# Optimization experiments

Measured on AMD Instinct MI355X. Metric: run time of the kernel, lower is better.

## Reference

```python
import jax, jax.numpy as jnp
import numpy as np

B, S, D = 8, 2048, 512
FF = 2048
E = 8

def setup_inputs() -> dict:
    key = jax.random.key(0)
    ks = jax.random.split(key, 7)
    s = 1.0 / np.sqrt(D)
    sf = 1.0 / np.sqrt(FF)
    return {
        "x":  jax.random.normal(ks[0], (B, S, D), dtype=jnp.float32),
        "Wg": jax.random.uniform(ks[1], (D, E), jnp.float32, -s, s),
        "bg": jax.random.uniform(ks[2], (E,), jnp.float32, -s, s),
        "W1": jax.random.uniform(ks[3], (E, D, FF), jnp.float32, -s, s),
        "b1": jax.random.uniform(ks[4], (E, FF), jnp.float32, -s, s),
        "W2": jax.random.uniform(ks[5], (E, FF, D), jnp.float32, -sf, sf),
        "b2": jax.random.uniform(ks[6], (E, D), jnp.float32, -sf, sf),
    }

def reference(x, Wg, bg, W1, b1, W2, b2):
    b, s, d = x.shape
    xf = x.reshape(-1, d)                      # [T, D]
    logits = xf @ Wg + bg                      # [T, E]
    probs = jax.nn.softmax(logits, axis=-1)
    pmax = jnp.max(probs, axis=-1)             # [T]
    routes = jnp.argmax(probs, axis=-1)        # [T] int
    xs = xf * pmax[:, None]                    # scale tokens by router prob
    # per-expert FFN over all tokens, select the routed expert's output
    out_tok = jnp.zeros_like(xf)
    for e in range(E):
        h = jax.nn.relu(xs @ W1[e] + b1[e])    # [T, FF]
        y = h @ W2[e] + b2[e]                  # [T, D]
        out_tok = jnp.where((routes == e)[:, None], y, out_tok)
    # torch.cat of per-expert nonzero-index gathers == tokens stably sorted by expert id
    order = jnp.argsort(routes)                # jnp.argsort is stable
    return out_tok[order].reshape(b, s, d)
```

## Files before the change

kernel.cpp:

```cpp
#include <hip/hip_runtime.h>
#include <hip/hip_bf16.h>

constexpr int TTOK  = 16384;
constexpr int DDIM  = 512;
constexpr int FFDIM = 2048;
constexpr int NEXP  = 8;
constexpr int GB_TOK = 16;
constexpr int NGB    = TTOK / GB_TOK;
constexpr int MAXTILES = TTOK / 128 + NEXP;

typedef __attribute__((ext_vector_type(8))) short short8_t;
typedef __attribute__((ext_vector_type(4))) float f32x4_t;

__device__ __forceinline__ unsigned short f2bf(float f) {
    union { float f; unsigned u; } v; v.f = f;
    return (unsigned short)((v.u + 0x7fffu + ((v.u >> 16) & 1u)) >> 16);
}

__device__ __forceinline__ void gl_lds16(const void* g, void* l) {
    __builtin_amdgcn_global_load_lds(
        (const __attribute__((address_space(1))) void*)g,
        (__attribute__((address_space(3))) void*)l,
        16, 0, 0);
}

__global__ __launch_bounds__(256) void transpose_cvt2(const float* __restrict__ W1,
                                                      const float* __restrict__ W2,
                                                      unsigned short* __restrict__ W1T,
                                                      unsigned short* __restrict__ W2T) {
    __shared__ float tile[32][33];
    int z = blockIdx.z;
    bool isW2 = z >= NEXP;
    int e = isW2 ? z - NEXP : z;
    int R = isW2 ? FFDIM : DDIM;
    int C = isW2 ? DDIM : FFDIM;
    int tilesC = C / 32;
    int t = blockIdx.x;
    int c0 = (t % tilesC) * 32;
    int r0 = (t / tilesC) * 32;
    const float* s = (isW2 ? W2 : W1) + (size_t)e * DDIM * FFDIM;
    unsigned short* d = (isW2 ? W2T : W1T) + (size_t)e * DDIM * FFDIM;
    int tx = threadIdx.x & 31, ty = threadIdx.x >> 5;
    #pragma unroll
    for (int i = 0; i < 4; i++)
        tile[ty + 8 * i][tx] = s[(size_t)(r0 + ty + 8 * i) * C + c0 + tx];
    __syncthreads();
    #pragma unroll
    for (int i = 0; i < 4; i++)
        d[(size_t)(c0 + ty + 8 * i) * R + r0 + tx] = f2bf(tile[tx][ty + 8 * i]);
}

__global__ __launch_bounds__(256) void gate_kernel(const float* __restrict__ x,
                                                   const float* __restrict__ Wg,
                                                   const float* __restrict__ bg,
                                                   int* __restrict__ route,
                                                   float* __restrict__ pmax,
                                                   int* __restrict__ blockCounts) {
    __shared__ int cnt[NEXP];
    __shared__ float bgs[NEXP];
    int tid = threadIdx.x;
    if (tid < NEXP) { cnt[tid] = 0; bgs[tid] = bg[tid]; }
    __syncthreads();
    int wave = tid >> 6, lane = tid & 63;
    float w[8][8];
    #pragma unroll
    for (int jj = 0; jj < 8; jj++) {
        float4 a = *(const float4*)(Wg + (size_t)(lane * 8 + jj) * NEXP);
        float4 b = *(const float4*)(Wg + (size_t)(lane * 8 + jj) * NEXP + 4);
        w[jj][0] = a.x; w[jj][1] = a.y; w[jj][2] = a.z; w[jj][3] = a.w;
        w[jj][4] = b.x; w[jj][5] = b.y; w[jj][6] = b.z; w[jj][7] = b.w;
    }
    int tbase = blockIdx.x * GB_TOK + wave * 4;
    for (int it = 0; it < 4; it++) {
        int t = tbase + it;
        float4 xa = *(const float4*)(x + (size_t)t * DDIM + lane * 8);
        float4 xb = *(const float4*)(x + (size_t)t * DDIM + lane * 8 + 4);
        float xs[8] = {xa.x, xa.y, xa.z, xa.w, xb.x, xb.y, xb.z, xb.w};
        double acc[NEXP];
        #pragma unroll
        for (int e = 0; e < NEXP; e++) acc[e] = 0.0;
        #pragma unroll
        for (int jj = 0; jj < 8; jj++) {
            double xv = (double)xs[jj];
            #pragma unroll
            for (int e = 0; e < NEXP; e++) acc[e] += xv * (double)w[jj][e];
        }
        #pragma unroll
        for (int off = 32; off > 0; off >>= 1) {
            #pragma unroll
            for (int e = 0; e < NEXP; e++) acc[e] += __shfl_down(acc[e], off);
        }
        if (lane == 0) {
            double l[NEXP];
            #pragma unroll
            for (int e = 0; e < NEXP; e++) l[e] = acc[e] + (double)bgs[e];
            int r = 0; double lm = l[0];
            #pragma unroll
            for (int e = 1; e < NEXP; e++) if (l[e] > lm) { lm = l[e]; r = e; }
            double s = 0.0;
            #pragma unroll
            for (int e = 0; e < NEXP; e++) s += exp(l[e] - lm);
            route[t] = r;
            pmax[t] = (float)(1.0 / s);
            atomicAdd(&cnt[r], 1);
        }
    }
    __syncthreads();
    if (tid < NEXP) blockCounts[blockIdx.x * NEXP + tid] = cnt[tid];
}

__global__ __launch_bounds__(1024) void scan_kernel(const int* __restrict__ blockCounts,
                                                    int* __restrict__ blockOffsets,
                                                    int* __restrict__ segPrefix,
                                                    int* __restrict__ tilePrefix) {
    __shared__ int sc[NGB][NEXP];
    __shared__ int base[NEXP + 1];
    int b = threadIdx.x;
    int c[NEXP];
    #pragma unroll
    for (int e = 0; e < NEXP; e++) { c[e] = blockCounts[b * NEXP + e]; sc[b][e] = c[e]; }
    __syncthreads();
    for (int off = 1; off < NGB; off <<= 1) {
        int t[NEXP];
        if (b >= off) {
            #pragma unroll
            for (int e = 0; e < NEXP; e++) t[e] = sc[b - off][e];
        }
        __syncthreads();
        if (b >= off) {
            #pragma unroll
            for (int e = 0; e < NEXP; e++) sc[b][e] += t[e];
        }
        __syncthreads();
    }
    if (b == 0) {
        int s = 0;
        #pragma unroll
        for (int e = 0; e < NEXP; e++) { base[e] = s; s += sc[NGB - 1][e]; }
        base[NEXP] = s;
        for (int e = 0; e <= NEXP; e++) segPrefix[e] = base[e];
        int tp = 0;
        tilePrefix[0] = 0;
        for (int e = 0; e < NEXP; e++) {
            tp += (sc[NGB - 1][e] + 127) / 128;
            tilePrefix[e + 1] = tp;
        }
    }
    __syncthreads();
    #pragma unroll
    for (int e = 0; e < NEXP; e++)
        blockOffsets[b * NEXP + e] = base[e] + sc[b][e] - c[e];
}

__global__ __launch_bounds__(256) void scatter_kernel(const float* __restrict__ x,
                                                      const int* __restrict__ route,
                                                      const float* __restrict__ pmax,
                                                      const int* __restrict__ blockOffsets,
                                                      unsigned short* __restrict__ Xs) {
    __shared__ int dstL[GB_TOK];
    __shared__ float pmL[GB_TOK];
    int tid = threadIdx.x;
    int bb = blockIdx.x;
    if (tid < GB_TOK) {
        int t = bb * GB_TOK + tid;
        int r = route[t];
        unsigned long long ltmask = (tid == 0) ? 0ull : ((~0ull) >> (64 - tid));
        int rank = 0;
        #pragma unroll
        for (int e = 0; e < NEXP; e++) {
            unsigned long long m = __ballot(r == e);
            if (r == e) rank = __popcll(m & ltmask);
        }
        dstL[tid] = blockOffsets[bb * NEXP + r] + rank;
        pmL[tid] = pmax[t];
    }
    __syncthreads();
    int wave = tid >> 6, lane = tid & 63;
    for (int rr = 0; rr < 4; rr++) {
        int rowl = wave * 4 + rr;
        int t = bb * GB_TOK + rowl;
        float pm = pmL[rowl];
        const float4* xr = (const float4*)(x + (size_t)t * DDIM) + lane * 2;
        float4 a = xr[0], b = xr[1];
        union { short8_t v; unsigned short s[8]; } o;
        o.s[0] = f2bf(a.x * pm); o.s[1] = f2bf(a.y * pm);
        o.s[2] = f2bf(a.z * pm); o.s[3] = f2bf(a.w * pm);
        o.s[4] = f2bf(b.x * pm); o.s[5] = f2bf(b.y * pm);
        o.s[6] = f2bf(b.z * pm); o.s[7] = f2bf(b.w * pm);
        *(short8_t*)(Xs + (size_t)dstL[rowl] * DDIM + lane * 8) = o.v;
    }
}

template <bool RELU, typename OutT, int K, int N>
__global__ __launch_bounds__(256) void gemm_seg(const unsigned short* __restrict__ A,
                                                const unsigned short* __restrict__ Bt,
                                                const float* __restrict__ bias,
                                                OutT* __restrict__ C,
                                                const int* __restrict__ segPrefix,
                                                const int* __restrict__ tilePrefix) {
    int t = blockIdx.x;
    if (t >= tilePrefix[NEXP]) return;
    int e = 0;
    #pragma unroll
    for (int i = 1; i <= NEXP; i++) e += (t >= tilePrefix[i]) ? 1 : 0;
    int seg1 = segPrefix[e + 1];
    int m0 = segPrefix[e] + (t - tilePrefix[e]) * 128;
    int n0 = blockIdx.y * 128;

    __shared__ unsigned short As[2 * 4096];
    __shared__ unsigned short Bs[2 * 4096];

    int tid = threadIdx.x, wave = tid >> 6, lane = tid & 63;
    const unsigned short* Bte = Bt + (size_t)e * N * K;

    int srow = lane >> 2;
    int sg   = (lane & 3) ^ ((lane >> 2) & 3) ^ ((lane >> 4) & 3);
    int scol = sg * 8;

    f32x4_t acc[4][4];
    #pragma unroll
    for (int i = 0; i < 4; i++)
        #pragma unroll
        for (int j = 0; j < 4; j++) acc[i][j] = (f32x4_t){0.f, 0.f, 0.f, 0.f};

    int wm = (wave & 1) * 64;
    int wn = (wave >> 1) * 64;
    int frow = lane & 15;
    int gr = lane >> 4;
    int fswz = (gr ^ (frow & 3) ^ ((frow >> 2) & 3)) * 8;

    int reg0 = wave * 2;
    int arow0 = m0 + reg0 * 16 + srow;
    arow0 = arow0 < TTOK ? arow0 : TTOK - 1;
    int arow1 = m0 + (reg0 + 1) * 16 + srow;
    arow1 = arow1 < TTOK ? arow1 : TTOK - 1;
    const unsigned short* aptr0 = A + (size_t)arow0 * K + scol;
    const unsigned short* aptr1 = A + (size_t)arow1 * K + scol;
    const unsigned short* bptr0 = Bte + (size_t)(n0 + reg0 * 16 + srow) * K + scol;
    const unsigned short* bptr1 = Bte + (size_t)(n0 + (reg0 + 1) * 16 + srow) * K + scol;

    #pragma unroll
    for (int kc = 0; kc < K; kc += 64) {
        #pragma unroll
        for (int p = 0; p < 2; p++) {
            gl_lds16(aptr0 + kc + p * 32, &As[p * 4096 + reg0 * 512]);
            gl_lds16(aptr1 + kc + p * 32, &As[p * 4096 + (reg0 + 1) * 512]);
            gl_lds16(bptr0 + kc + p * 32, &Bs[p * 4096 + reg0 * 512]);
            gl_lds16(bptr1 + kc + p * 32, &Bs[p * 4096 + (reg0 + 1) * 512]);
        }
        __syncthreads();
        #pragma unroll
        for (int p = 0; p < 2; p++) {
            short8_t af[4], bfr[4];
            #pragma unroll
            for (int i = 0; i < 4; i++)
                af[i] = *(const short8_t*)&As[p * 4096 + (wm + i * 16 + frow) * 32 + fswz];
            #pragma unroll
            for (int j = 0; j < 4; j++)
                bfr[j] = *(const short8_t*)&Bs[p * 4096 + (wn + j * 16 + frow) * 32 + fswz];
            #pragma unroll
            for (int i = 0; i < 4; i++)
                #pragma unroll
                for (int j = 0; j < 4; j++)
                    acc[i][j] = __builtin_amdgcn_mfma_f32_16x16x32_bf16(af[i], bfr[j], acc[i][j], 0, 0, 0);
        }
        __syncthreads();
    }

    int quad = lane >> 4;
    int colb = lane & 15;
    float bv[4];
    #pragma unroll
    for (int j = 0; j < 4; j++) bv[j] = bias[(size_t)e * N + n0 + wn + j * 16 + colb];

    if constexpr (sizeof(OutT) == 2) {
        unsigned short* cbuf = As;
        #pragma unroll
        for (int p = 0; p < 2; p++) {
            __syncthreads();
            if ((wave >> 1) == p) {
                #pragma unroll
                for (int i = 0; i < 4; i++)
                    #pragma unroll
                    for (int j = 0; j < 4; j++)
                        #pragma unroll
                        for (int r = 0; r < 4; r++) {
                            float v = acc[i][j][r] + bv[j];
                            if (RELU) v = fmaxf(v, 0.0f);
                            cbuf[(wm + i * 16 + quad * 4 + r) * 72 + j * 16 + colb] = f2bf(v);
                        }
            }
            __syncthreads();
            int row = tid >> 1, ch = (tid & 1) * 32;
            int grow = m0 + row;
            if (grow < seg1) {
                #pragma unroll
                for (int k = 0; k < 4; k++) {
                    short8_t v = *(const short8_t*)&cbuf[row * 72 + ch + k * 8];
                    *(short8_t*)&C[(size_t)grow * N + n0 + p * 64 + ch + k * 8] = v;
                }
            }
        }
    } else {
        #pragma unroll
        for (int i = 0; i < 4; i++) {
            #pragma unroll
            for (int j = 0; j < 4; j++) {
                int col = n0 + wn + j * 16 + colb;
                #pragma unroll
                for (int r = 0; r < 4; r++) {
                    int row = m0 + wm + i * 16 + quad * 4 + r;
                    if (row < seg1) {
                        float v = acc[i][j][r] + bv[j];
                        if (RELU) v = fmaxf(v, 0.0f);
                        C[(size_t)row * N + col] = v;
                    }
                }
            }
        }
    }
}

extern "C" void kernel_launch(void* const* d_in, const int* in_sizes, int n_in,
                              void* d_out, int out_size, void* d_ws, size_t ws_size,
                              hipStream_t stream) {
    const float* x  = (const float*)d_in[0];
    const float* Wg = (const float*)d_in[1];
    const float* bg = (const float*)d_in[2];
    const float* W1 = (const float*)d_in[3];
    const float* b1 = (const float*)d_in[4];
    const float* W2 = (const float*)d_in[5];
    const float* b2 = (const float*)d_in[6];
    float* out = (float*)d_out;

    char* ws = (char*)d_ws;
    size_t off = 0;
    auto alloc = [&](size_t bytes) -> char* {
        char* p = ws + off;
        off += (bytes + 255) & ~(size_t)255;
        return p;
    };
    unsigned short* W1T = (unsigned short*)alloc((size_t)NEXP * DDIM * FFDIM * 2);
    unsigned short* W2T = (unsigned short*)alloc((size_t)NEXP * DDIM * FFDIM * 2);
    unsigned short* Xs  = (unsigned short*)alloc((size_t)TTOK * DDIM * 2);
    unsigned short* H   = (unsigned short*)alloc((size_t)TTOK * FFDIM * 2);
    int*   route        = (int*)alloc((size_t)TTOK * 4);
    float* pmaxArr      = (float*)alloc((size_t)TTOK * 4);
    int*   blockCounts  = (int*)alloc((size_t)NGB * NEXP * 4);
    int*   blockOffsets = (int*)alloc((size_t)NGB * NEXP * 4);
    int*   segPrefix    = (int*)alloc((size_t)(NEXP + 1) * 4);
    int*   tilePrefix   = (int*)alloc((size_t)(NEXP + 1) * 4);

    transpose_cvt2<<<dim3(1024, 1, 2 * NEXP), 256, 0, stream>>>(W1, W2, W1T, W2T);
    gate_kernel<<<NGB, 256, 0, stream>>>(x, Wg, bg, route, pmaxArr, blockCounts);
    scan_kernel<<<1, NGB, 0, stream>>>(blockCounts, blockOffsets, segPrefix, tilePrefix);
    scatter_kernel<<<NGB, 256, 0, stream>>>(x, route, pmaxArr, blockOffsets, Xs);
    gemm_seg<true, unsigned short, DDIM, FFDIM><<<dim3(MAXTILES, FFDIM / 128, 1), 256, 0, stream>>>(
        Xs, W1T, b1, H, segPrefix, tilePrefix);
    gemm_seg<false, float, FFDIM, DDIM><<<dim3(MAXTILES, DDIM / 128, 1), 256, 0, stream>>>(
        H, W2T, b2, out, segPrefix, tilePrefix);
}
```

Measured before the change: 311.5 us.

## Double-buffer LDS tiles in expert GEMM, swizzle tile order and epilogue LDS

Doubles the shared-memory A/B buffers so the next K-chunk is loaded via global_load_lds while the current chunk feeds the MFMAs. This leaves one barrier per iteration instead of two and is meant to hide global load latency. It also remaps blockIdx.x to interleave tiles across groups of eight, and XOR-swizzles the bf16 epilogue staging buffer to cut LDS bank conflicts. LDS use per block doubles to 64 KB, which may lower occupancy. The async LDS loads are not explicitly waited on before the barrier, so correctness relies on the compiler inserting the waits.

```diff
diff --git a/kernel.cpp b/kernel.cpp
--- a/kernel.cpp
+++ b/kernel.cpp
@@ -198,7 +198,9 @@
                                                 OutT* __restrict__ C,
                                                 const int* __restrict__ segPrefix,
                                                 const int* __restrict__ tilePrefix) {
-    int t = blockIdx.x;
+    int bx = blockIdx.x;
+    bx = (bx & 7) * (MAXTILES / 8) + (bx >> 3);
+    int t = bx;
     if (t >= tilePrefix[NEXP]) return;
     int e = 0;
     #pragma unroll
@@ -207,8 +209,8 @@
     int m0 = segPrefix[e] + (t - tilePrefix[e]) * 128;
     int n0 = blockIdx.y * 128;
 
-    __shared__ unsigned short As[2 * 4096];
-    __shared__ unsigned short Bs[2 * 4096];
+    __shared__ unsigned short As[2 * 8192];
+    __shared__ unsigned short Bs[2 * 8192];
 
     int tid = threadIdx.x, wave = tid >> 6, lane = tid & 63;
     const unsigned short* Bte = Bt + (size_t)e * N * K;
@@ -239,33 +241,44 @@
     const unsigned short* bptr0 = Bte + (size_t)(n0 + reg0 * 16 + srow) * K + scol;
     const unsigned short* bptr1 = Bte + (size_t)(n0 + (reg0 + 1) * 16 + srow) * K + scol;
 
-    #pragma unroll
-    for (int kc = 0; kc < K; kc += 64) {
+    auto stage = [&](int buf, int kc) {
+        int lb = buf * 8192 + reg0 * 512;
         #pragma unroll
         for (int p = 0; p < 2; p++) {
-            gl_lds16(aptr0 + kc + p * 32, &As[p * 4096 + reg0 * 512]);
-            gl_lds16(aptr1 + kc + p * 32, &As[p * 4096 + (reg0 + 1) * 512]);
-            gl_lds16(bptr0 + kc + p * 32, &Bs[p * 4096 + reg0 * 512]);
-            gl_lds16(bptr1 + kc + p * 32, &Bs[p * 4096 + (reg0 + 1) * 512]);
-        }
-        __syncthreads();
+            gl_lds16(aptr0 + kc + p * 32, &As[lb + p * 4096]);
+            gl_lds16(aptr1 + kc + p * 32, &As[lb + p * 4096 + 512]);
+            gl_lds16(bptr0 + kc + p * 32, &Bs[lb + p * 4096]);
+            gl_lds16(bptr1 + kc + p * 32, &Bs[lb + p * 4096 + 512]);
+        }
+    };
+    auto compute = [&](int buf) {
         #pragma unroll
         for (int p = 0; p < 2; p++) {
             short8_t af[4], bfr[4];
             #pragma unroll
             for (int i = 0; i < 4; i++)
-                af[i] = *(const short8_t*)&As[p * 4096 + (wm + i * 16 + frow) * 32 + fswz];
+                af[i] = *(const short8_t*)&As[buf * 8192 + p * 4096 + (wm + i * 16 + frow) * 32 + fswz];
             #pragma unroll
             for (int j = 0; j < 4; j++)
-                bfr[j] = *(const short8_t*)&Bs[p * 4096 + (wn + j * 16 + frow) * 32 + fswz];
+                bfr[j] = *(const short8_t*)&Bs[buf * 8192 + p * 4096 + (wn + j * 16 + frow) * 32 + fswz];
             #pragma unroll
             for (int i = 0; i < 4; i++)
                 #pragma unroll
                 for (int j = 0; j < 4; j++)
                     acc[i][j] = __builtin_amdgcn_mfma_f32_16x16x32_bf16(af[i], bfr[j], acc[i][j], 0, 0, 0);
         }
+    };
+
+    constexpr int NK = K / 64;
+    stage(0, 0);
+    __syncthreads();
+    #pragma unroll 2
+    for (int tk = 0; tk < NK - 1; ++tk) {
+        stage((tk + 1) & 1, (tk + 1) * 64);
+        compute(tk & 1);
         __syncthreads();
     }
+    compute((NK - 1) & 1);
 
     int quad = lane >> 4;
     int colb = lane & 15;
@@ -287,7 +300,9 @@
                         for (int r = 0; r < 4; r++) {
                             float v = acc[i][j][r] + bv[j];
                             if (RELU) v = fmaxf(v, 0.0f);
-                            cbuf[(wm + i * 16 + quad * 4 + r) * 72 + j * 16 + colb] = f2bf(v);
+                            int wrow = wm + i * 16 + quad * 4 + r;
+                            int cc = (j * 16 + colb) ^ (((wrow >> 3) & 1) * 16);
+                            cbuf[wrow * 72 + cc] = f2bf(v);
                         }
             }
             __syncthreads();
@@ -296,7 +311,8 @@
             if (grow < seg1) {
                 #pragma unroll
                 for (int k = 0; k < 4; k++) {
-                    short8_t v = *(const short8_t*)&cbuf[row * 72 + ch + k * 8];
+                    int vv = (ch + k * 8) ^ (((row >> 3) & 1) * 16);
+                    short8_t v = *(const short8_t*)&cbuf[row * 72 + vv];
                     *(short8_t*)&C[(size_t)grow * N + n0 + p * 64 + ch + k * 8] = v;
                 }
             }
```

Measured after the change: 341.6 us. 1.1x slower.

## Add 256x256 eight-wave pipelined GEMM kernel for first expert FFN layer

Applied to the files above, without the earlier changes.

Replaces the first grouped GEMM (X·W1 with ReLU) with a new kernel using 256x256 tiles, 512 threads, direct global-to-LDS loads, and a four-phase double-buffered schedule that interleaves LDS loads with MFMA blocks under barriers and raised wave priority. It adds a second tile prefix for 256-row tiles and remaps block indices so that work is interleaved across expert tiles, applying the same remap to the remaining 128-tile GEMM. The larger tiles raise operand reuse and cut global traffic, but they waste more work on padded tail tiles per expert and use a large LDS footprint that limits occupancy. The bf16 epilogue branch is removed from the generic GEMM, since it now only produces fp32 output.

```diff
diff --git a/kernel.cpp b/kernel.cpp
--- a/kernel.cpp
+++ b/kernel.cpp
@@ -8,6 +8,7 @@
 constexpr int GB_TOK = 16;
 constexpr int NGB    = TTOK / GB_TOK;
 constexpr int MAXTILES = TTOK / 128 + NEXP;
+constexpr int MT256    = TTOK / 256 + NEXP;
 
 typedef __attribute__((ext_vector_type(8))) short short8_t;
 typedef __attribute__((ext_vector_type(4))) float f32x4_t;
@@ -112,7 +113,8 @@
 __global__ __launch_bounds__(1024) void scan_kernel(const int* __restrict__ blockCounts,
                                                     int* __restrict__ blockOffsets,
                                                     int* __restrict__ segPrefix,
-                                                    int* __restrict__ tilePrefix) {
+                                                    int* __restrict__ tilePrefix,
+                                                    int* __restrict__ tilePrefix2) {
     __shared__ int sc[NGB][NEXP];
     __shared__ int base[NEXP + 1];
     int b = threadIdx.x;
@@ -139,11 +141,13 @@
         for (int e = 0; e < NEXP; e++) { base[e] = s; s += sc[NGB - 1][e]; }
         base[NEXP] = s;
         for (int e = 0; e <= NEXP; e++) segPrefix[e] = base[e];
-        int tp = 0;
-        tilePrefix[0] = 0;
+        int tp = 0, tp2 = 0;
+        tilePrefix[0] = 0; tilePrefix2[0] = 0;
         for (int e = 0; e < NEXP; e++) {
-            tp += (sc[NGB - 1][e] + 127) / 128;
+            tp  += (sc[NGB - 1][e] + 127) / 128;
+            tp2 += (sc[NGB - 1][e] + 255) / 256;
             tilePrefix[e + 1] = tp;
+            tilePrefix2[e + 1] = tp2;
         }
     }
     __syncthreads();
@@ -191,6 +195,164 @@
     }
 }
 
+__global__ __launch_bounds__(512, 2) void gemm1_8ph(const unsigned short* __restrict__ A,
+                                                    const unsigned short* __restrict__ Bt,
+                                                    const float* __restrict__ bias,
+                                                    unsigned short* __restrict__ C,
+                                                    const int* __restrict__ segPrefix,
+                                                    const int* __restrict__ tileP2) {
+    constexpr int K = 512, N = 2048, NK = K / 64;
+    int bx = blockIdx.x;
+    bx = (bx & 7) * (MT256 / 8) + (bx >> 3);
+    if (bx >= tileP2[NEXP]) return;
+    int e = 0;
+    #pragma unroll
+    for (int i = 1; i <= NEXP; i++) e += (bx >= tileP2[i]) ? 1 : 0;
+    int seg1 = segPrefix[e + 1];
+    int m0 = segPrefix[e] + (bx - tileP2[e]) * 256;
+    int n0 = blockIdx.y * 256;
+
+    __shared__ __align__(16) unsigned short SH[65536];
+
+    int tid = threadIdx.x, wave = tid >> 6, lane = tid & 63;
+    int wm = wave >> 2, wn = wave & 3;
+    int frow = lane & 15, gr = lane >> 4;
+    const unsigned short* Bte = Bt + (size_t)e * N * K;
+
+    const unsigned short* aS[2][2];
+    const unsigned short* bS[2][2];
+    #pragma unroll
+    for (int r = 0; r < 2; r++) {
+        int q = wave * 2 + r;
+        int Lr = q * 1024 + lane * 16;
+        int rh = Lr >> 7;
+        int cb = (Lr & 127) ^ (((Lr >> 9) & 1) << 5);
+        #pragma unroll
+        for (int h = 0; h < 2; h++) {
+            int arow = m0 + h * 128 + rh; arow = arow < TTOK ? arow : TTOK - 1;
+            aS[h][r] = A + (size_t)arow * K + (cb >> 1);
+            bS[h][r] = Bte + (size_t)(n0 + h * 128 + rh) * K + (cb >> 1);
+        }
+    }
+
+    f32x4_t acc[8][4];
+    #pragma unroll
+    for (int i = 0; i < 8; i++)
+        #pragma unroll
+        for (int j = 0; j < 4; j++) acc[i][j] = (f32x4_t){0.f, 0.f, 0.f, 0.f};
+
+    short8_t aR[4][2];
+    short8_t bR[2][2][2];
+
+    auto BAR = [] {
+        asm volatile("" ::: "memory");
+        __builtin_amdgcn_s_barrier();
+        asm volatile("" ::: "memory");
+    };
+    auto stA = [&](int bufd, int h, int kc) {
+        #pragma unroll
+        for (int r = 0; r < 2; r++)
+            gl_lds16(aS[h][r] + kc, &SH[(bufd * 2 + h) * 8192 + (wave * 2 + r) * 512]);
+    };
+    auto stB = [&](int bufd, int h, int kc) {
+        #pragma unroll
+        for (int r = 0; r < 2; r++)
+            gl_lds16(bS[h][r] + kc, &SH[32768 + (bufd * 2 + h) * 8192 + (wave * 2 + r) * 512]);
+    };
+    auto off = [&](int buf, int h, int rh, int ks) {
+        int b = rh * 128 + ks * 64 + gr * 16;
+        b ^= ((b >> 9) & 1) << 5;
+        return (buf * 2 + h) * 8192 + (b >> 1);
+    };
+    auto ldA = [&](int buf, int ih) {
+        #pragma unroll
+        for (int i4 = 0; i4 < 4; i4++)
+            #pragma unroll
+            for (int ks = 0; ks < 2; ks++)
+                aR[i4][ks] = *(const short8_t*)&SH[off(buf, ih, wm * 64 + i4 * 16 + frow, ks)];
+    };
+    auto ldB = [&](int buf, int jh) {
+        #pragma unroll
+        for (int jq = 0; jq < 2; jq++)
+            #pragma unroll
+            for (int ks = 0; ks < 2; ks++)
+                bR[jh][jq][ks] = *(const short8_t*)&SH[32768 + off(buf, jh, wn * 32 + jq * 16 + frow, ks)];
+    };
+    auto mm = [&](int ih, int jh) {
+        __builtin_amdgcn_s_setprio(1);
+        #pragma unroll
+        for (int i4 = 0; i4 < 4; i4++)
+            #pragma unroll
+            for (int jq = 0; jq < 2; jq++)
+                #pragma unroll
+                for (int ks = 0; ks < 2; ks++)
+                    acc[ih * 4 + i4][jh * 2 + jq] = __builtin_amdgcn_mfma_f32_16x16x32_bf16(
+                        aR[i4][ks], bR[jh][jq][ks], acc[ih * 4 + i4][jh * 2 + jq], 0, 0, 0);
+        __builtin_amdgcn_s_setprio(0);
+    };
+
+    stA(0, 0, 0); stB(0, 1, 0); stA(0, 1, 0); stB(0, 0, 0);
+    stA(1, 0, 64); stB(1, 1, 64);
+    asm volatile("s_waitcnt vmcnt(4)" ::: "memory");
+    BAR();
+
+    #pragma unroll 2
+    for (int t = 0; t < NK; ++t) {
+        const int bc = t & 1;
+        ldA(bc, 0); ldB(bc, 0);
+        if (t + 1 < NK) stA(bc ^ 1, 1, (t + 1) * 64);
+        BAR(); mm(0, 0); BAR();
+        ldB(bc, 1);
+        if (t + 1 < NK) stB(bc ^ 1, 0, (t + 1) * 64);
+        BAR(); mm(0, 1); BAR();
+        ldA(bc, 1);
+        if (t + 2 < NK) stA(bc, 0, (t + 2) * 64);
+        BAR(); mm(1, 1); BAR();
+        if (t + 2 < NK) stB(bc, 1, (t + 2) * 64);
+        BAR(); mm(1, 0);
+        if (t + 1 < NK) {
+            if (t + 2 < NK) asm volatile("s_waitcnt vmcnt(4)" ::: "memory");
+            else            asm volatile("s_waitcnt vmcnt(0)" ::: "memory");
+        }
+        BAR();
+    }
+
+    float bvv[2][2];
+    #pragma unroll
+    for (int jh = 0; jh < 2; jh++)
+        #pragma unroll
+        for (int jq = 0; jq < 2; jq++)
+            bvv[jh][jq] = bias[(size_t)e * N + n0 + jh * 128 + wn * 32 + jq * 16 + frow];
+
+    unsigned short* cbuf = SH;
+    #pragma unroll
+    for (int p = 0; p < 2; p++) {
+        __syncthreads();
+        #pragma unroll
+        for (int i = 0; i < 8; i++)
+            #pragma unroll
+            for (int jq = 0; jq < 2; jq++)
+                #pragma unroll
+                for (int rr = 0; rr < 4; rr++) {
+                    int row = (i >> 2) * 128 + wm * 64 + (i & 3) * 16 + gr * 4 + rr;
+                    int col = wn * 32 + jq * 16 + frow;
+                    float v = acc[i][p * 2 + jq][rr] + bvv[p][jq];
+                    v = fmaxf(v, 0.0f);
+                    cbuf[row * 136 + col] = f2bf(v);
+                }
+        __syncthreads();
+        int row = tid >> 1, part = tid & 1;
+        int grow = m0 + row;
+        if (grow < seg1) {
+            #pragma unroll
+            for (int c = 0; c < 8; c++) {
+                short8_t v = *(const short8_t*)&cbuf[row * 136 + part * 64 + c * 8];
+                *(short8_t*)&C[(size_t)grow * N + n0 + p * 128 + part * 64 + c * 8] = v;
+            }
+        }
+    }
+}
+
 template <bool RELU, typename OutT, int K, int N>
 __global__ __launch_bounds__(256) void gemm_seg(const unsigned short* __restrict__ A,
                                                 const unsigned short* __restrict__ Bt,
@@ -198,7 +360,9 @@
                                                 OutT* __restrict__ C,
                                                 const int* __restrict__ segPrefix,
                                                 const int* __restrict__ tilePrefix) {
-    int t = blockIdx.x;
+    int bx = blockIdx.x;
+    bx = (bx & 7) * (MAXTILES / 8) + (bx >> 3);
+    int t = bx;
     if (t >= tilePrefix[NEXP]) return;
     int e = 0;
     #pragma unroll
@@ -273,48 +437,18 @@
     #pragma unroll
     for (int j = 0; j < 4; j++) bv[j] = bias[(size_t)e * N + n0 + wn + j * 16 + colb];
 
-    if constexpr (sizeof(OutT) == 2) {
-        unsigned short* cbuf = As;
-        #pragma unroll
-        for (int p = 0; p < 2; p++) {
-            __syncthreads();
-            if ((wave >> 1) == p) {
-                #pragma unroll
-                for (int i = 0; i < 4; i++)
-                    #pragma unroll
-                    for (int j = 0; j < 4; j++)
-                        #pragma unroll
-                        for (int r = 0; r < 4; r++) {
-                            float v = acc[i][j][r] + bv[j];
-                            if (RELU) v = fmaxf(v, 0.0f);
-                            cbuf[(wm + i * 16 + quad * 4 + r) * 72 + j * 16 + colb] = f2bf(v);
-                        }
-            }
-            __syncthreads();
-            int row = tid >> 1, ch = (tid & 1) * 32;
-            int grow = m0 + row;
-            if (grow < seg1) {
-                #pragma unroll
-                for (int k = 0; k < 4; k++) {
-                    short8_t v = *(const short8_t*)&cbuf[row * 72 + ch + k * 8];
-                    *(short8_t*)&C[(size_t)grow * N + n0 + p * 64 + ch + k * 8] = v;
-                }
-            }
-        }
-    } else {
-        #pragma unroll
-        for (int i = 0; i < 4; i++) {
-            #pragma unroll
-            for (int j = 0; j < 4; j++) {
-                int col = n0 + wn + j * 16 + colb;
-                #pragma unroll
-                for (int r = 0; r < 4; r++) {
-                    int row = m0 + wm + i * 16 + quad * 4 + r;
-                    if (row < seg1) {
-                        float v = acc[i][j][r] + bv[j];
-                        if (RELU) v = fmaxf(v, 0.0f);
-                        C[(size_t)row * N + col] = v;
-                    }
+    #pragma unroll
+    for (int i = 0; i < 4; i++) {
+        #pragma unroll
+        for (int j = 0; j < 4; j++) {
+            int col = n0 + wn + j * 16 + colb;
+            #pragma unroll
+            for (int r = 0; r < 4; r++) {
+                int row = m0 + wm + i * 16 + quad * 4 + r;
+                if (row < seg1) {
+                    float v = acc[i][j][r] + bv[j];
+                    if (RELU) v = fmaxf(v, 0.0f);
+                    C[(size_t)row * N + col] = v;
                 }
             }
         }
@@ -350,13 +484,14 @@
     int*   blockOffsets = (int*)alloc((size_t)NGB * NEXP * 4);
     int*   segPrefix    = (int*)alloc((size_t)(NEXP + 1) * 4);
     int*   tilePrefix   = (int*)alloc((size_t)(NEXP + 1) * 4);
+    int*   tilePrefix2  = (int*)alloc((size_t)(NEXP + 1) * 4);
 
     transpose_cvt2<<<dim3(1024, 1, 2 * NEXP), 256, 0, stream>>>(W1, W2, W1T, W2T);
     gate_kernel<<<NGB, 256, 0, stream>>>(x, Wg, bg, route, pmaxArr, blockCounts);
-    scan_kernel<<<1, NGB, 0, stream>>>(blockCounts, blockOffsets, segPrefix, tilePrefix);
+    scan_kernel<<<1, NGB, 0, stream>>>(blockCounts, blockOffsets, segPrefix, tilePrefix, tilePrefix2);
     scatter_kernel<<<NGB, 256, 0, stream>>>(x, route, pmaxArr, blockOffsets, Xs);
-    gemm_seg<true, unsigned short, DDIM, FFDIM><<<dim3(MAXTILES, FFDIM / 128, 1), 256, 0, stream>>>(
-        Xs, W1T, b1, H, segPrefix, tilePrefix);
+    gemm1_8ph<<<dim3(MT256, FFDIM / 256, 1), 512, 0, stream>>>(
+        Xs, W1T, b1, H, segPrefix, tilePrefix2);
     gemm_seg<false, float, FFDIM, DDIM><<<dim3(MAXTILES, DDIM / 128, 1), 256, 0, stream>>>(
         H, W2T, b2, out, segPrefix, tilePrefix);
 }
```

Result: no change. 310.3 us (-0.4%).
